# Kernel tuning notes

Hardware: AMD Instinct MI355X
Metric: run time of the kernel (lower is better)

## Reference

```python
import jax, jax.numpy as jnp
import numpy as np

IN_FEATURES = 256
GROWTH = 32
EPS = 1e-5
N, C_TOTAL, H, W = 32, IN_FEATURES + GROWTH, 56, 56


def setup_inputs() -> dict:
    key = jax.random.key(0)
    ks = jax.random.split(key, 6)
    all_features = jax.random.normal(ks[0], (N, C_TOTAL, H, W), dtype=jnp.float32)
    bn_weight = jax.random.uniform(ks[1], (IN_FEATURES,), jnp.float32, 0.5, 1.5)
    bn_bias = jax.random.normal(ks[2], (IN_FEATURES,), jnp.float32) * 0.1
    running_mean = jax.random.normal(ks[3], (IN_FEATURES,), jnp.float32) * 0.1
    running_var = jax.random.uniform(ks[4], (IN_FEATURES,), jnp.float32, 0.5, 1.5)
    # kaiming_uniform_(a=sqrt(5)) -> bound = 1/sqrt(fan_in), fan_in = in*3*3
    bound = 1.0 / np.sqrt(IN_FEATURES * 9)
    conv_weight = jax.random.uniform(ks[5], (GROWTH, IN_FEATURES, 3, 3), jnp.float32, -bound, bound)
    return {
        "all_features": all_features,
        "bn_weight": bn_weight,
        "bn_bias": bn_bias,
        "running_mean": running_mean,
        "running_var": running_var,
        "conv_weight": conv_weight,
        "out_channel_offset": IN_FEATURES,
    }


def reference(all_features, bn_weight, bn_bias, running_mean, running_var, conv_weight, out_channel_offset):
    # Fold BN: y = x * scale + shift, then ReLU, then 3x3 SAME conv (no bias),
    # writing the growth_rate output channels into the shared concat buffer.
    scale = bn_weight * jax.lax.rsqrt(running_var + EPS)          # [C_in]
    shift = bn_bias - running_mean * scale                        # [C_in]
    x = all_features[:, :IN_FEATURES]                             # [N, C_in, H, W]
    y = jax.nn.relu(x * scale[None, :, None, None] + shift[None, :, None, None])
    out = jax.lax.conv_general_dilated(
        y, conv_weight, window_strides=(1, 1), padding="SAME",
        dimension_numbers=("NCHW", "OIHW", "NCHW"))               # [N, growth, H, W]
    return all_features.at[:, out_channel_offset:out_channel_offset + GROWTH].set(out)
```

## Files before the change

kernel.cpp:

```cpp
#include <hip/hip_runtime.h>

typedef short short8 __attribute__((ext_vector_type(8)));
typedef float f32x4 __attribute__((ext_vector_type(4)));

#define N_IMG 32
#define C_IN  256
#define C_OUT 32
#define HWDIM 56
#define C_TOT 288
#define EPSV  1e-5f
#define PLANE (HWDIM * HWDIM)
#define CHW   (C_TOT * PLANE)

#define YP    58
#define YROW  (YP * C_IN)
#define YIMG  (YP * YROW)
#define YWS_ELEMS ((size_t)N_IMG * YIMG)
#define WT_ELEMS  (9 * C_OUT * C_IN)
#define WS_NEED   (YWS_ELEMS * 2 + (size_t)WT_ELEMS * 2)

static __device__ __forceinline__ unsigned short f2bf(float f) {
    union { float f; unsigned u; } v; v.f = f;
    unsigned r = (v.u + 0x7FFFu + ((v.u >> 16) & 1u)) >> 16;
    return (unsigned short)r;
}

__global__ __launch_bounds__(256) void prep_kernel(const float* __restrict__ cw,
                                                   unsigned short* __restrict__ yws,
                                                   unsigned short* __restrict__ wt) {
    int b = blockIdx.x, t = threadIdx.x;
    if (b < 912) {
        int gid = b * 256 + t;
        int px = gid >> 5, ch = gid & 31;
        int n = px / 228, r = px % 228;
        int hh, ww;
        if (r < 58)       { hh = 0;        ww = r;       }
        else if (r < 116) { hh = 57;       ww = r - 58;  }
        else if (r < 172) { hh = r - 115;  ww = 0;       }
        else              { hh = r - 171;  ww = 57;      }
        uint4 z = {0u, 0u, 0u, 0u};
        *(uint4*)((char*)yws + ((size_t)n * YIMG + (size_t)hh * YROW + (size_t)ww * C_IN) * 2 + ch * 16) = z;
    } else {
        int id  = (b - 912) * 256 + t;
        int tap = id >> 13;
        int oc  = (id >> 8) & 31;
        int ic  = id & 255;
        wt[id] = f2bf(cw[(oc * C_IN + ic) * 9 + tap]);
    }
}

__global__ __launch_bounds__(256) void bn_relu_pack(const float* __restrict__ xin,
                                                    const float* __restrict__ bnw,
                                                    const float* __restrict__ bnb,
                                                    const float* __restrict__ rmean,
                                                    const float* __restrict__ rvar,
                                                    float* __restrict__ out,
                                                    unsigned short* __restrict__ yws) {
    __shared__ float s_scale[C_IN], s_shift[C_IN];
    __shared__ unsigned short s_y[HWDIM * 264 + 8];

    int h = blockIdx.x, n = blockIdx.y, t = threadIdx.x;
    {
        float sc = bnw[t] * rsqrtf(rvar[t] + EPSV);
        s_scale[t] = sc;
        s_shift[t] = bnb[t] - rmean[t] * sc;
    }
    __syncthreads();

    const size_t nb = (size_t)n * CHW + (size_t)h * HWDIM;
    #pragma unroll
    for (int i = 0; i < 14; ++i) {
        int id = i * 256 + t;
        int c = id / 14, wq = id - c * 14;
        const float* gp = xin + nb + (size_t)c * PLANE + wq * 4;
        float4 x = *(const float4*)gp;
        *(float4*)(out + nb + (size_t)c * PLANE + wq * 4) = x;
        float sc = s_scale[c], sh = s_shift[c];
        int wb = wq * 4;
        s_y[(wb + 0) * 264 + c] = f2bf(fmaxf(fmaf(x.x, sc, sh), 0.f));
        s_y[(wb + 1) * 264 + c] = f2bf(fmaxf(fmaf(x.y, sc, sh), 0.f));
        s_y[(wb + 2) * 264 + c] = f2bf(fmaxf(fmaf(x.z, sc, sh), 0.f));
        s_y[(wb + 3) * 264 + c] = f2bf(fmaxf(fmaf(x.w, sc, sh), 0.f));
    }
    __syncthreads();

    unsigned short* ybase = yws + (size_t)n * YIMG + (size_t)(h + 1) * YROW + C_IN;
    #pragma unroll
    for (int i = 0; i < 7; ++i) {
        int id = i * 256 + t;
        int px = id >> 5, co = (id & 31) * 8;
        uint4 v = *(uint4*)((char*)s_y + ((size_t)px * 264 + co) * 2);
        *(uint4*)((char*)ybase + ((size_t)px * C_IN + co) * 2) = v;
    }
}

__global__ __launch_bounds__(256) void conv_mfma(const unsigned short* __restrict__ yws,
                                                 const unsigned short* __restrict__ wt,
                                                 float* __restrict__ out) {
    __shared__ char s_wt[16384];

    int b0 = blockIdx.x;
    int bid = (b0 & 7) * 112 + (b0 >> 3);
    int n = bid / 28, h0 = (bid - n * 28) * 2;

    int t = threadIdx.x, lane = t & 63, wv = t >> 6;
    int l15 = lane & 15, koct = lane >> 4;
    int pt0 = wv * 2, pt1 = (wv < 3) ? wv * 2 + 1 : 6;

    int px0 = pt0 * 16 + l15, px1 = pt1 * 16 + l15;
    int r0 = px0 >= 56, w0 = px0 - 56 * r0;
    int r1 = px1 >= 56, w1 = px1 - 56 * r1;

    const char* ybase = (const char*)yws + (size_t)n * YIMG * 2;
    int po0 = ((h0 + r0) * YP + w0) * 512 + koct * 16;
    int po1 = ((h0 + r1) * YP + w1) * 512 + koct * 16;

    f32x4 acc[2][2] = {};
    int swz = (l15 & 7) << 4;

    for (int tap = 0; tap < 9; ++tap) {
        __syncthreads();
        #pragma unroll
        for (int i = 0; i < 4; ++i) {
            int id = i * 256 + t;
            int oc = id >> 5, icb = id & 31;
            uint4 v = *(const uint4*)(wt + tap * 8192 + oc * 256 + icb * 8);
            *(uint4*)(s_wt + oc * 512 + ((icb * 16) ^ ((oc & 7) << 4))) = v;
        }
        __syncthreads();

        int kh = tap / 3, kw = tap - kh * 3;
        int toff = (kh * YP + kw) * 512;

        #pragma unroll
        for (int c = 0; c < 8; ++c) {
            int aoff = (c * 64 + koct * 16) ^ swz;
            short8 a0 = *(short8*)(s_wt + l15 * 512 + aoff);
            short8 a1 = *(short8*)(s_wt + 8192 + l15 * 512 + aoff);
            short8 b0v = *(const short8*)(ybase + po0 + toff + c * 64);
            short8 b1v = *(const short8*)(ybase + po1 + toff + c * 64);
            acc[0][0] = __builtin_amdgcn_mfma_f32_16x16x32_bf16(a0, b0v, acc[0][0], 0, 0, 0);
            acc[1][0] = __builtin_amdgcn_mfma_f32_16x16x32_bf16(a1, b0v, acc[1][0], 0, 0, 0);
            acc[0][1] = __builtin_amdgcn_mfma_f32_16x16x32_bf16(a0, b1v, acc[0][1], 0, 0, 0);
            acc[1][1] = __builtin_amdgcn_mfma_f32_16x16x32_bf16(a1, b1v, acc[1][1], 0, 0, 0);
        }
    }

    float* ob = out + (size_t)n * CHW + (size_t)C_IN * PLANE + (size_t)h0 * HWDIM;
    #pragma unroll
    for (int oct = 0; oct < 2; ++oct) {
        #pragma unroll
        for (int p = 0; p < 2; ++p) {
            if (p == 1 && wv == 3) continue;
            int rr = p ? r1 : r0, wc = p ? w1 : w0;
            #pragma unroll
            for (int j = 0; j < 4; ++j) {
                int oc = oct * 16 + koct * 4 + j;
                ob[(size_t)oc * PLANE + rr * HWDIM + wc] = acc[oct][p][j];
            }
        }
    }
}

__global__ __launch_bounds__(256) void fused_bn_relu_conv(
    const float* __restrict__ xin, const float* __restrict__ bnw,
    const float* __restrict__ bnb, const float* __restrict__ rmean,
    const float* __restrict__ rvar, const float* __restrict__ cw,
    float* __restrict__ out)
{
    __shared__ float s_scale[C_IN];
    __shared__ float s_shift[C_IN];
    __shared__ float s_y[3][32][60];

    const int h = blockIdx.x, n = blockIdx.y, t = threadIdx.x;
    {
        float sc = bnw[t] * rsqrtf(rvar[t] + EPSV);
        s_scale[t] = sc;
        s_shift[t] = bnb[t] - rmean[t] * sc;
    }
    const int oc = t >> 3;
    const int w0 = (t & 7) * 7;
    float acc[7];
    #pragma unroll
    for (int j = 0; j < 7; ++j) acc[j] = 0.f;
    const size_t nbase = (size_t)n * CHW;

    for (int cb = 0; cb < 8; ++cb) {
        __syncthreads();
        for (int idx = t; idx < 3 * 32 * 15; idx += 256) {
            int r = idx / 480, rem = idx - r * 480;
            int ic = rem / 15, s = rem - ic * 15;
            int icg = (cb << 5) + ic, hr = h - 1 + r;
            if (s < 14) {
                float4 x = make_float4(0.f, 0.f, 0.f, 0.f);
                bool inb = (unsigned)hr < HWDIM;
                if (inb) {
                    const float* gp = xin + nbase + (size_t)icg * PLANE + hr * HWDIM + (s << 2);
                    x = *reinterpret_cast<const float4*>(gp);
                    if (r == 1) {
                        float* op = out + nbase + (size_t)icg * PLANE + h * HWDIM + (s << 2);
                        *reinterpret_cast<float4*>(op) = x;
                    }
                }
                float sc = s_scale[icg], sh = s_shift[icg];
                int e = (s << 2) + 1;
                s_y[r][ic][e + 0] = inb ? fmaxf(fmaf(x.x, sc, sh), 0.f) : 0.f;
                s_y[r][ic][e + 1] = inb ? fmaxf(fmaf(x.y, sc, sh), 0.f) : 0.f;
                s_y[r][ic][e + 2] = inb ? fmaxf(fmaf(x.z, sc, sh), 0.f) : 0.f;
                s_y[r][ic][e + 3] = inb ? fmaxf(fmaf(x.w, sc, sh), 0.f) : 0.f;
            } else {
                s_y[r][ic][0] = 0.f; s_y[r][ic][57] = 0.f;
            }
        }
        __syncthreads();
        const float* wbase = cw + ((size_t)oc * C_IN + (cb << 5)) * 9;
        #pragma unroll 2
        for (int ic = 0; ic < 32; ++ic) {
            const float* wp = wbase + ic * 9;
            float wk[9];
            #pragma unroll
            for (int k = 0; k < 9; ++k) wk[k] = wp[k];
            #pragma unroll
            for (int r = 0; r < 3; ++r) {
                float yy[9];
                #pragma unroll
                for (int j = 0; j < 9; ++j) yy[j] = s_y[r][ic][w0 + j];
                #pragma unroll
                for (int kw = 0; kw < 3; ++kw) {
                    float wv2 = wk[r * 3 + kw];
                    #pragma unroll
                    for (int j = 0; j < 7; ++j)
                        acc[j] = fmaf(yy[j + kw], wv2, acc[j]);
                }
            }
        }
    }
    float* op = out + nbase + (size_t)(C_IN + oc) * PLANE + h * HWDIM + w0;
    #pragma unroll
    for (int j = 0; j < 7; ++j) op[j] = acc[j];
}

extern "C" void kernel_launch(void* const* d_in, const int* in_sizes, int n_in,
                              void* d_out, int out_size, void* d_ws, size_t ws_size,
                              hipStream_t stream) {
    const float* xin = (const float*)d_in[0];
    const float* bnw = (const float*)d_in[1];
    const float* bnb = (const float*)d_in[2];
    const float* rm  = (const float*)d_in[3];
    const float* rv  = (const float*)d_in[4];
    const float* cwt = (const float*)d_in[5];
    float* out = (float*)d_out;

    if (ws_size < WS_NEED) {
        dim3 grid(HWDIM, N_IMG);
        fused_bn_relu_conv<<<grid, 256, 0, stream>>>(xin, bnw, bnb, rm, rv, cwt, out);
        return;
    }

    unsigned short* yws = (unsigned short*)d_ws;
    unsigned short* wtb = yws + YWS_ELEMS;

    prep_kernel<<<1200, 256, 0, stream>>>(cwt, yws, wtb);
    bn_relu_pack<<<dim3(HWDIM, N_IMG), 256, 0, stream>>>(xin, bnw, bnb, rm, rv, out, yws);
    conv_mfma<<<896, 256, 0, stream>>>(yws, wtb, out);
}
```

Before: 329.8 us.

## Double-buffer conv weight tiles, pre-swizzle weights, and rework BN pack kernel layout

The conv kernel now double-buffers the per-tap weight tile in LDS, loading the next tap's weights into registers while the current tap's MFMAs run. This leaves one barrier per tap instead of two. Weights are pre-swizzled in the prep kernel so the LDS copy is a straight linear store, and all eight B fragments are loaded before each tap's MFMA loop. The BN/ReLU pack kernel moves to 1024 threads with a channel-major LDS staging layout and 2-byte scattered global stores, which may coalesce worse. The small-workspace fallback path is removed.

```diff
diff --git a/kernel.cpp b/kernel.cpp
--- a/kernel.cpp
+++ b/kernel.cpp
@@ -43,24 +43,27 @@
     } else {
         int id  = (b - 912) * 256 + t;
         int tap = id >> 13;
-        int oc  = (id >> 8) & 31;
-        int ic  = id & 255;
+        int pos = id & 8191;
+        int g   = pos >> 3, r = pos & 7;
+        int oc  = g >> 5;
+        int icb = (g & 31) ^ (oc & 7);
+        int ic  = icb * 8 + r;
         wt[id] = f2bf(cw[(oc * C_IN + ic) * 9 + tap]);
     }
 }
 
-__global__ __launch_bounds__(256) void bn_relu_pack(const float* __restrict__ xin,
-                                                    const float* __restrict__ bnw,
-                                                    const float* __restrict__ bnb,
-                                                    const float* __restrict__ rmean,
-                                                    const float* __restrict__ rvar,
-                                                    float* __restrict__ out,
-                                                    unsigned short* __restrict__ yws) {
+__global__ __launch_bounds__(1024) void bn_relu_pack(const float* __restrict__ xin,
+                                                     const float* __restrict__ bnw,
+                                                     const float* __restrict__ bnb,
+                                                     const float* __restrict__ rmean,
+                                                     const float* __restrict__ rvar,
+                                                     float* __restrict__ out,
+                                                     unsigned short* __restrict__ yws) {
     __shared__ float s_scale[C_IN], s_shift[C_IN];
-    __shared__ unsigned short s_y[HWDIM * 264 + 8];
+    __shared__ unsigned short s_yc[C_IN * 66];
 
     int h = blockIdx.x, n = blockIdx.y, t = threadIdx.x;
-    {
+    if (t < C_IN) {
         float sc = bnw[t] * rsqrtf(rvar[t] + EPSV);
         s_scale[t] = sc;
         s_shift[t] = bnb[t] - rmean[t] * sc;
@@ -69,35 +72,39 @@
 
     const size_t nb = (size_t)n * CHW + (size_t)h * HWDIM;
     #pragma unroll
-    for (int i = 0; i < 14; ++i) {
-        int id = i * 256 + t;
-        int c = id / 14, wq = id - c * 14;
-        const float* gp = xin + nb + (size_t)c * PLANE + wq * 4;
-        float4 x = *(const float4*)gp;
-        *(float4*)(out + nb + (size_t)c * PLANE + wq * 4) = x;
-        float sc = s_scale[c], sh = s_shift[c];
-        int wb = wq * 4;
-        s_y[(wb + 0) * 264 + c] = f2bf(fmaxf(fmaf(x.x, sc, sh), 0.f));
-        s_y[(wb + 1) * 264 + c] = f2bf(fmaxf(fmaf(x.y, sc, sh), 0.f));
-        s_y[(wb + 2) * 264 + c] = f2bf(fmaxf(fmaf(x.z, sc, sh), 0.f));
-        s_y[(wb + 3) * 264 + c] = f2bf(fmaxf(fmaf(x.w, sc, sh), 0.f));
+    for (int i = 0; i < 4; ++i) {
+        int id = i * 1024 + t;
+        if (id < 3584) {
+            int c = id / 14, wq = id - c * 14;
+            const float* gp = xin + nb + (size_t)c * PLANE + wq * 4;
+            float4 x = *(const float4*)gp;
+            *(float4*)(out + nb + (size_t)c * PLANE + wq * 4) = x;
+            float sc = s_scale[c], sh = s_shift[c];
+            unsigned p0 = (unsigned)f2bf(fmaxf(fmaf(x.x, sc, sh), 0.f))
+                        | ((unsigned)f2bf(fmaxf(fmaf(x.y, sc, sh), 0.f)) << 16);
+            unsigned p1 = (unsigned)f2bf(fmaxf(fmaf(x.z, sc, sh), 0.f))
+                        | ((unsigned)f2bf(fmaxf(fmaf(x.w, sc, sh), 0.f)) << 16);
+            *(unsigned*)(&s_yc[c * 66 + 4 * wq])     = p0;
+            *(unsigned*)(&s_yc[c * 66 + 4 * wq + 2]) = p1;
+        }
     }
     __syncthreads();
 
     unsigned short* ybase = yws + (size_t)n * YIMG + (size_t)(h + 1) * YROW + C_IN;
     #pragma unroll
     for (int i = 0; i < 7; ++i) {
-        int id = i * 256 + t;
-        int px = id >> 5, co = (id & 31) * 8;
-        uint4 v = *(uint4*)((char*)s_y + ((size_t)px * 264 + co) * 2);
-        *(uint4*)((char*)ybase + ((size_t)px * C_IN + co) * 2) = v;
+        int id = i * 1024 + t;
+        int c = id & 255, pq = id >> 8;
+        unsigned v = *(const unsigned*)(&s_yc[c * 66 + 2 * pq]);
+        ybase[(size_t)(2 * pq)     * C_IN + c] = (unsigned short)(v & 0xFFFFu);
+        ybase[(size_t)(2 * pq + 1) * C_IN + c] = (unsigned short)(v >> 16);
     }
 }
 
 __global__ __launch_bounds__(256) void conv_mfma(const unsigned short* __restrict__ yws,
                                                  const unsigned short* __restrict__ wt,
                                                  float* __restrict__ out) {
-    __shared__ char s_wt[16384];
+    __shared__ unsigned short s_wt[2][8192];
 
     int b0 = blockIdx.x;
     int bid = (b0 & 7) * 112 + (b0 >> 3);
@@ -114,130 +121,82 @@
     const char* ybase = (const char*)yws + (size_t)n * YIMG * 2;
     int po0 = ((h0 + r0) * YP + w0) * 512 + koct * 16;
     int po1 = ((h0 + r1) * YP + w1) * 512 + koct * 16;
-
-    f32x4 acc[2][2] = {};
     int swz = (l15 & 7) << 4;
 
+    {
+        uint4 st0, st1, st2, st3;
+        st0 = *(const uint4*)(wt + (0 * 256 + t) * 8);
+        st1 = *(const uint4*)(wt + (1 * 256 + t) * 8);
+        st2 = *(const uint4*)(wt + (2 * 256 + t) * 8);
+        st3 = *(const uint4*)(wt + (3 * 256 + t) * 8);
+        *(uint4*)((char*)s_wt[0] + (0 * 256 + t) * 16) = st0;
+        *(uint4*)((char*)s_wt[0] + (1 * 256 + t) * 16) = st1;
+        *(uint4*)((char*)s_wt[0] + (2 * 256 + t) * 16) = st2;
+        *(uint4*)((char*)s_wt[0] + (3 * 256 + t) * 16) = st3;
+    }
+    __syncthreads();
+
+    f32x4 acc00 = {}, acc01 = {}, acc10 = {}, acc11 = {};
+
+    #pragma unroll
     for (int tap = 0; tap < 9; ++tap) {
-        __syncthreads();
+        const int cur = tap & 1;
+
+        uint4 nt0, nt1, nt2, nt3;
+        if (tap < 8) {
+            const unsigned short* g = wt + (size_t)(tap + 1) * 8192;
+            nt0 = *(const uint4*)(g + (0 * 256 + t) * 8);
+            nt1 = *(const uint4*)(g + (1 * 256 + t) * 8);
+            nt2 = *(const uint4*)(g + (2 * 256 + t) * 8);
+            nt3 = *(const uint4*)(g + (3 * 256 + t) * 8);
+        }
+
+        int kh = tap / 3, kw = tap - kh * 3;
+        const char* yb0 = ybase + po0 + (kh * YP + kw) * 512;
+        const char* yb1 = ybase + po1 + (kh * YP + kw) * 512;
+
+        short8 B0[8], B1[8];
         #pragma unroll
-        for (int i = 0; i < 4; ++i) {
-            int id = i * 256 + t;
-            int oc = id >> 5, icb = id & 31;
-            uint4 v = *(const uint4*)(wt + tap * 8192 + oc * 256 + icb * 8);
-            *(uint4*)(s_wt + oc * 512 + ((icb * 16) ^ ((oc & 7) << 4))) = v;
-        }
-        __syncthreads();
-
-        int kh = tap / 3, kw = tap - kh * 3;
-        int toff = (kh * YP + kw) * 512;
-
+        for (int c = 0; c < 8; ++c) {
+            B0[c] = *(const short8*)(yb0 + c * 64);
+            B1[c] = *(const short8*)(yb1 + c * 64);
+        }
+
+        const char* sw = (const char*)s_wt[cur];
         #pragma unroll
         for (int c = 0; c < 8; ++c) {
             int aoff = (c * 64 + koct * 16) ^ swz;
-            short8 a0 = *(short8*)(s_wt + l15 * 512 + aoff);
-            short8 a1 = *(short8*)(s_wt + 8192 + l15 * 512 + aoff);
-            short8 b0v = *(const short8*)(ybase + po0 + toff + c * 64);
-            short8 b1v = *(const short8*)(ybase + po1 + toff + c * 64);
-            acc[0][0] = __builtin_amdgcn_mfma_f32_16x16x32_bf16(a0, b0v, acc[0][0], 0, 0, 0);
-            acc[1][0] = __builtin_amdgcn_mfma_f32_16x16x32_bf16(a1, b0v, acc[1][0], 0, 0, 0);
-            acc[0][1] = __builtin_amdgcn_mfma_f32_16x16x32_bf16(a0, b1v, acc[0][1], 0, 0, 0);
-            acc[1][1] = __builtin_amdgcn_mfma_f32_16x16x32_bf16(a1, b1v, acc[1][1], 0, 0, 0);
-        }
+            short8 a0 = *(const short8*)(sw + l15 * 512 + aoff);
+            short8 a1 = *(const short8*)(sw + 8192 + l15 * 512 + aoff);
+            acc00 = __builtin_amdgcn_mfma_f32_16x16x32_bf16(a0, B0[c], acc00, 0, 0, 0);
+            acc10 = __builtin_amdgcn_mfma_f32_16x16x32_bf16(a1, B0[c], acc10, 0, 0, 0);
+            acc01 = __builtin_amdgcn_mfma_f32_16x16x32_bf16(a0, B1[c], acc01, 0, 0, 0);
+            acc11 = __builtin_amdgcn_mfma_f32_16x16x32_bf16(a1, B1[c], acc11, 0, 0, 0);
+        }
+
+        if (tap < 8) {
+            char* dw = (char*)s_wt[cur ^ 1];
+            *(uint4*)(dw + (0 * 256 + t) * 16) = nt0;
+            *(uint4*)(dw + (1 * 256 + t) * 16) = nt1;
+            *(uint4*)(dw + (2 * 256 + t) * 16) = nt2;
+            *(uint4*)(dw + (3 * 256 + t) * 16) = nt3;
+        }
+        __syncthreads();
     }
 
     float* ob = out + (size_t)n * CHW + (size_t)C_IN * PLANE + (size_t)h0 * HWDIM;
-    #pragma unroll
-    for (int oct = 0; oct < 2; ++oct) {
+    {
         #pragma unroll
-        for (int p = 0; p < 2; ++p) {
-            if (p == 1 && wv == 3) continue;
-            int rr = p ? r1 : r0, wc = p ? w1 : w0;
-            #pragma unroll
-            for (int j = 0; j < 4; ++j) {
-                int oc = oct * 16 + koct * 4 + j;
-                ob[(size_t)oc * PLANE + rr * HWDIM + wc] = acc[oct][p][j];
+        for (int j = 0; j < 4; ++j) {
+            int oc0 = koct * 4 + j;
+            ob[(size_t)oc0 * PLANE + r0 * HWDIM + w0]        = acc00[j];
+            ob[(size_t)(16 + oc0) * PLANE + r0 * HWDIM + w0] = acc10[j];
+            if (wv < 3) {
+                ob[(size_t)oc0 * PLANE + r1 * HWDIM + w1]        = acc01[j];
+                ob[(size_t)(16 + oc0) * PLANE + r1 * HWDIM + w1] = acc11[j];
             }
         }
     }
-}
-
-__global__ __launch_bounds__(256) void fused_bn_relu_conv(
-    const float* __restrict__ xin, const float* __restrict__ bnw,
-    const float* __restrict__ bnb, const float* __restrict__ rmean,
-    const float* __restrict__ rvar, const float* __restrict__ cw,
-    float* __restrict__ out)
-{
-    __shared__ float s_scale[C_IN];
-    __shared__ float s_shift[C_IN];
-    __shared__ float s_y[3][32][60];
-
-    const int h = blockIdx.x, n = blockIdx.y, t = threadIdx.x;
-    {
-        float sc = bnw[t] * rsqrtf(rvar[t] + EPSV);
-        s_scale[t] = sc;
-        s_shift[t] = bnb[t] - rmean[t] * sc;
-    }
-    const int oc = t >> 3;
-    const int w0 = (t & 7) * 7;
-    float acc[7];
-    #pragma unroll
-    for (int j = 0; j < 7; ++j) acc[j] = 0.f;
-    const size_t nbase = (size_t)n * CHW;
-
-    for (int cb = 0; cb < 8; ++cb) {
-        __syncthreads();
-        for (int idx = t; idx < 3 * 32 * 15; idx += 256) {
-            int r = idx / 480, rem = idx - r * 480;
-            int ic = rem / 15, s = rem - ic * 15;
-            int icg = (cb << 5) + ic, hr = h - 1 + r;
-            if (s < 14) {
-                float4 x = make_float4(0.f, 0.f, 0.f, 0.f);
-                bool inb = (unsigned)hr < HWDIM;
-                if (inb) {
-                    const float* gp = xin + nbase + (size_t)icg * PLANE + hr * HWDIM + (s << 2);
-                    x = *reinterpret_cast<const float4*>(gp);
-                    if (r == 1) {
-                        float* op = out + nbase + (size_t)icg * PLANE + h * HWDIM + (s << 2);
-                        *reinterpret_cast<float4*>(op) = x;
-                    }
-                }
-                float sc = s_scale[icg], sh = s_shift[icg];
-                int e = (s << 2) + 1;
-                s_y[r][ic][e + 0] = inb ? fmaxf(fmaf(x.x, sc, sh), 0.f) : 0.f;
-                s_y[r][ic][e + 1] = inb ? fmaxf(fmaf(x.y, sc, sh), 0.f) : 0.f;
-                s_y[r][ic][e + 2] = inb ? fmaxf(fmaf(x.z, sc, sh), 0.f) : 0.f;
-                s_y[r][ic][e + 3] = inb ? fmaxf(fmaf(x.w, sc, sh), 0.f) : 0.f;
-            } else {
-                s_y[r][ic][0] = 0.f; s_y[r][ic][57] = 0.f;
-            }
-        }
-        __syncthreads();
-        const float* wbase = cw + ((size_t)oc * C_IN + (cb << 5)) * 9;
-        #pragma unroll 2
-        for (int ic = 0; ic < 32; ++ic) {
-            const float* wp = wbase + ic * 9;
-            float wk[9];
-            #pragma unroll
-            for (int k = 0; k < 9; ++k) wk[k] = wp[k];
-            #pragma unroll
-            for (int r = 0; r < 3; ++r) {
-                float yy[9];
-                #pragma unroll
-                for (int j = 0; j < 9; ++j) yy[j] = s_y[r][ic][w0 + j];
-                #pragma unroll
-                for (int kw = 0; kw < 3; ++kw) {
-                    float wv2 = wk[r * 3 + kw];
-                    #pragma unroll
-                    for (int j = 0; j < 7; ++j)
-                        acc[j] = fmaf(yy[j + kw], wv2, acc[j]);
-                }
-            }
-        }
-    }
-    float* op = out + nbase + (size_t)(C_IN + oc) * PLANE + h * HWDIM + w0;
-    #pragma unroll
-    for (int j = 0; j < 7; ++j) op[j] = acc[j];
 }
 
 extern "C" void kernel_launch(void* const* d_in, const int* in_sizes, int n_in,
@@ -251,16 +210,10 @@
     const float* cwt = (const float*)d_in[5];
     float* out = (float*)d_out;
 
-    if (ws_size < WS_NEED) {
-        dim3 grid(HWDIM, N_IMG);
-        fused_bn_relu_conv<<<grid, 256, 0, stream>>>(xin, bnw, bnb, rm, rv, cwt, out);
-        return;
-    }
-
     unsigned short* yws = (unsigned short*)d_ws;
     unsigned short* wtb = yws + YWS_ELEMS;
 
     prep_kernel<<<1200, 256, 0, stream>>>(cwt, yws, wtb);
-    bn_relu_pack<<<dim3(HWDIM, N_IMG), 256, 0, stream>>>(xin, bnw, bnb, rm, rv, out, yws);
+    bn_relu_pack<<<dim3(HWDIM, N_IMG), 1024, 0, stream>>>(xin, bnw, bnb, rm, rv, out, yws);
     conv_mfma<<<896, 256, 0, stream>>>(yws, wtb, out);
 }
```

Result: no change. 327.1 us (-0.8%).
